# Performance work log

Hardware: AMD Instinct MI355X
Metric: run time of the kernel (lower is better)

## Reference

```python
import jax, jax.numpy as jnp
import numpy as np

P, Q, R = 3, 1, 0          # CliffordAlgebra(p=3, q=1, r=0)
N = P + Q + R
ALG = 1 << N               # 16 basis blades
SHIFTS = (1, 2, 4)


def _cayley():
    """Cayley table C[i,j,k]: blade_i * blade_j = C[i,j,i^j] * blade_{i^j}."""
    metric = [1.0] * P + [-1.0] * Q + [0.0] * R
    C = np.zeros((ALG, ALG, ALG), np.float32)
    for a in range(ALG):
        for b in range(ALG):
            x = a >> 1
            s = 0
            while x:                       # reordering sign
                s += bin(x & b).count('1')
                x >>= 1
            val = -1.0 if (s & 1) else 1.0
            for i in range(N):             # metric for repeated basis vectors
                if (a & b) >> i & 1:
                    val *= metric[i]
            C[a, b, a ^ b] = val
    return C

_C = _cayley()
C0 = jnp.asarray(_C[:, :, 0])                        # grade-0 slice: <a*b>_0
A = jnp.asarray((_C - _C.transpose(1, 0, 2)) / 2.0)  # antisym: (ab - ba)/2
VEC_MASK = jnp.asarray(np.array([1.0 if bin(i).count('1') == 1 else 0.0 for i in range(ALG)], np.float32))
BIV_MASK = jnp.asarray(np.array([1.0 if bin(i).count('1') == 2 else 0.0 for i in range(ALG)], np.float32))


def setup_inputs() -> dict:
    key = jax.random.key(0)
    k1, k2 = jax.random.split(key, 2)
    B, T, D = 8, 4096, 1024
    return {
        "x": jax.random.normal(k1, (B, T, D), jnp.float32),
        "gate_w": jax.random.normal(k2, (D, 1), jnp.float32) * 0.02,
        "gate_b": jnp.zeros((1,), jnp.float32),
        "scalar_weight": jnp.float32(0.5),
        "bivector_weight": jnp.float32(0.5),
    }


def reference(x, gate_w, gate_b, scalar_weight, bivector_weight):
    B, T, D = x.shape
    n = D // ALG                         # 64 chunks of 16 (D divisible, no pad)
    ss = jax.nn.sigmoid(scalar_weight)
    sb = jax.nn.sigmoid(bivector_weight)
    gate = jax.nn.sigmoid(x @ gate_w + gate_b)   # (B,T,1), gate of x (loop-invariant)
    xc = x.reshape(B, T, n, ALG)
    out = x
    for shift in SHIFTS:                 # T=4096 > shift always
        c = x - jnp.roll(x, shift, axis=1)
        cc = c.reshape(B, T, n, ALG)
        # inner product: scalar part per chunk, summed over chunks
        scalar = jnp.einsum('btni,btnj,ij->bt', xc, cc, C0)
        # wedge: antisymmetrized geometric product of vector-grade projections
        av = xc * VEC_MASK
        bv = cc * VEC_MASK
        wedge = jnp.einsum('btni,btnj,ijk->btnk', av, bv, A) * BIV_MASK
        delta = (sb * wedge).reshape(B, T, D)
        delta = delta.at[..., 0].add(ss * scalar)   # scalar_part lives at index 0
        out = out + gate * delta
    return out
```

## Files before the change

### kernel.cpp

```cpp
#include <hip/hip_runtime.h>
#include <math.h>


constexpr int T_DIM = 4096;
constexpr int D_DIM = 1024;

constexpr int QB0 = 0x8000;
constexpr int QB1 = 0x8055;
constexpr int QB2 = 0x80AA;

template <int PAT>
__device__ __forceinline__ float swz(float v) {
    return __int_as_float(__builtin_amdgcn_ds_swizzle(__float_as_int(v), PAT));
}

__device__ __forceinline__ float sigmoidf(float z) {
    return 1.0f / (1.0f + __expf(-z));
}

__global__ __launch_bounds__(256) void clifford_kernel(
    const float* __restrict__ x,
    const float* __restrict__ gate_w,
    const float* __restrict__ gate_b,
    const float* __restrict__ scalar_w,
    const float* __restrict__ bivec_w,
    float* __restrict__ out,
    int BT)
{
    int blk = blockIdx.x;
    if ((gridDim.x & 7) == 0) {
        const int per = gridDim.x >> 3;
        blk = (blockIdx.x & 7) * per + (blockIdx.x >> 3);
    }

    const int lane = threadIdx.x & 63;
    const int row  = blk * 4 + (threadIdx.x >> 6);
    if (row >= BT) return;
    const int b = row >> 12;
    const int t = row & (T_DIM - 1);
    const int sub = lane & 3;

    const float ss = sigmoidf(scalar_w[0]);
    const float sb = sigmoidf(bivec_w[0]);
    const float gb = gate_b[0];

    const float* __restrict__ r0 = x + (size_t)row * D_DIM;
    const size_t brow = (size_t)b * T_DIM;
    const float* __restrict__ r1 = x + (brow + ((t - 1) & (T_DIM - 1))) * D_DIM;
    const float* __restrict__ r2 = x + (brow + ((t - 2) & (T_DIM - 1))) * D_DIM;
    const float* __restrict__ r4 = x + (brow + ((t - 4) & (T_DIM - 1))) * D_DIM;

    float4 ws;
    if      (sub == 0) ws = make_float4( 1.f,  1.f,  1.f, -1.f);
    else if (sub == 1) ws = make_float4( 1.f, -1.f, -1.f, -1.f);
    else if (sub == 2) ws = make_float4(-1.f,  1.f,  1.f,  1.f);
    else               ws = make_float4( 1.f,  1.f,  1.f, -1.f);
    const float m3  = (sub == 0) ? 1.f : 0.f;
    const float a1  = (sub == 1) ? 1.f : 0.f;
    const float a2  = (sub == 2) ? 1.f : 0.f;
    const float m12 = (sub == 3) ? 1.f : 0.f;

    float4 xs[4], dl[4];
    float gate_part = 0.f, sc_part = 0.f;

    #pragma unroll
    for (int m = 0; m < 4; ++m) {
        const int off = (lane << 2) + (m << 8);
        const float4 xv = *(const float4*)(r0 + off);
        const float4 p1 = *(const float4*)(r1 + off);
        const float4 p2 = *(const float4*)(r2 + off);
        const float4 p4 = *(const float4*)(r4 + off);
        const float4 gv = *(const float4*)(gate_w + off);
        xs[m] = xv;

        float4 cs;
        cs.x = 3.f * xv.x - p1.x - p2.x - p4.x;
        cs.y = 3.f * xv.y - p1.y - p2.y - p4.y;
        cs.z = 3.f * xv.z - p1.z - p2.z - p4.z;
        cs.w = 3.f * xv.w - p1.w - p2.w - p4.w;

        gate_part += xv.x * gv.x + xv.y * gv.y + xv.z * gv.z + xv.w * gv.w;
        sc_part   += ws.x * (xv.x * cs.x) + ws.y * (xv.y * cs.y)
                   + ws.z * (xv.z * cs.z) + ws.w * (xv.w * cs.w);

        const float x1 = swz<QB0>(xv.y), x2 = swz<QB0>(xv.z);
        const float x4b = swz<QB1>(xv.x), x8b = swz<QB2>(xv.x);
        const float c1 = swz<QB0>(cs.y), c2 = swz<QB0>(cs.z);
        const float c4b = swz<QB1>(cs.x), c8b = swz<QB2>(cs.x);

        const float w3  = x1 * c2  - x2  * c1;
        const float w5  = x1 * c4b - x4b * c1;
        const float w6  = x2 * c4b - x4b * c2;
        const float w9  = x1 * c8b - x8b * c1;
        const float w10 = x2 * c8b - x8b * c2;
        const float w12 = x4b * c8b - x8b * c4b;

        dl[m] = make_float4(m12 * w12,
                            a1 * w5 + a2 * w9,
                            a1 * w6 + a2 * w10,
                            m3 * w3);
    }

    #pragma unroll
    for (int o = 32; o > 0; o >>= 1) {
        gate_part += __shfl_xor(gate_part, o, 64);
        sc_part   += __shfl_xor(sc_part,   o, 64);
    }
    const float gate = sigmoidf(gate_part + gb);
    const float gsb  = gate * sb;

    float* __restrict__ orow = out + (size_t)row * D_DIM;
    #pragma unroll
    for (int m = 0; m < 4; ++m) {
        float4 o4;
        o4.x = xs[m].x + gsb * dl[m].x;
        o4.y = xs[m].y + gsb * dl[m].y;
        o4.z = xs[m].z + gsb * dl[m].z;
        o4.w = xs[m].w + gsb * dl[m].w;
        if (m == 0 && lane == 0) o4.x += gate * ss * sc_part;
        *(float4*)(orow + (lane << 2) + (m << 8)) = o4;
    }
}

extern "C" void kernel_launch(void* const* d_in, const int* in_sizes, int n_in,
                              void* d_out, int out_size, void* d_ws, size_t ws_size,
                              hipStream_t stream) {
    const float* x  = (const float*)d_in[0];
    const float* gw = (const float*)d_in[1];
    const float* gb = (const float*)d_in[2];
    const float* sw = (const float*)d_in[3];
    const float* bw = (const float*)d_in[4];
    float* out = (float*)d_out;

    const int BT = in_sizes[0] / D_DIM;
    const int blocks = (BT + 3) / 4;
    hipLaunchKernelGGL(clifford_kernel, dim3(blocks), dim3(256), 0, stream,
                       x, gw, gb, sw, bw, out, BT);
}
```

Baseline: 244.9 us.

## Process several consecutive rows per wave with a register ring of prior rows

```diff
diff --git a/kernel.cpp b/kernel.cpp
--- a/kernel.cpp
+++ b/kernel.cpp
@@ -4,6 +4,7 @@
 
 constexpr int T_DIM = 4096;
 constexpr int D_DIM = 1024;
+constexpr int ROWS_PER_WAVE = 8;
 
 constexpr int QB0 = 0x8000;
 constexpr int QB1 = 0x8055;
@@ -18,7 +19,7 @@
     return 1.0f / (1.0f + __expf(-z));
 }
 
-__global__ __launch_bounds__(256) void clifford_kernel(
+__global__ __launch_bounds__(256, 3) void clifford_kernel(
     const float* __restrict__ x,
     const float* __restrict__ gate_w,
     const float* __restrict__ gate_b,
@@ -27,28 +28,34 @@
     float* __restrict__ out,
     int BT)
 {
-    int blk = blockIdx.x;
-    if ((gridDim.x & 7) == 0) {
-        const int per = gridDim.x >> 3;
-        blk = (blockIdx.x & 7) * per + (blockIdx.x >> 3);
+    const int lane = threadIdx.x & 63;
+    const int wid  = blockIdx.x * 4 + (threadIdx.x >> 6);
+    const int r0   = wid * ROWS_PER_WAVE;
+    if (r0 >= BT) return;
+    const int b  = r0 >> 12;
+    const int t0 = r0 & (T_DIM - 1);
+    const size_t brow = (size_t)b * T_DIM;
+    const int sub = lane & 3;
+
+    int off[4];
+    #pragma unroll
+    for (int m = 0; m < 4; ++m) off[m] = (lane << 2) + (m << 8);
+
+    float4 gw4[4];
+    #pragma unroll
+    for (int m = 0; m < 4; ++m) gw4[m] = *(const float4*)(gate_w + off[m]);
+
+    float4 ring[4][4];
+    #pragma unroll
+    for (int k = 1; k <= 4; ++k) {
+        const float* rp = x + (brow + ((t0 - k) & (T_DIM - 1))) * D_DIM;
+        #pragma unroll
+        for (int m = 0; m < 4; ++m) ring[4 - k][m] = *(const float4*)(rp + off[m]);
     }
-
-    const int lane = threadIdx.x & 63;
-    const int row  = blk * 4 + (threadIdx.x >> 6);
-    if (row >= BT) return;
-    const int b = row >> 12;
-    const int t = row & (T_DIM - 1);
-    const int sub = lane & 3;
 
     const float ss = sigmoidf(scalar_w[0]);
     const float sb = sigmoidf(bivec_w[0]);
     const float gb = gate_b[0];
-
-    const float* __restrict__ r0 = x + (size_t)row * D_DIM;
-    const size_t brow = (size_t)b * T_DIM;
-    const float* __restrict__ r1 = x + (brow + ((t - 1) & (T_DIM - 1))) * D_DIM;
-    const float* __restrict__ r2 = x + (brow + ((t - 2) & (T_DIM - 1))) * D_DIM;
-    const float* __restrict__ r4 = x + (brow + ((t - 4) & (T_DIM - 1))) * D_DIM;
 
     float4 ws;
     if      (sub == 0) ws = make_float4( 1.f,  1.f,  1.f, -1.f);
@@ -59,66 +66,82 @@
     const float a1  = (sub == 1) ? 1.f : 0.f;
     const float a2  = (sub == 2) ? 1.f : 0.f;
     const float m12 = (sub == 3) ? 1.f : 0.f;
+    const bool is_lane0 = (lane == 0);
 
-    float4 xs[4], dl[4];
-    float gate_part = 0.f, sc_part = 0.f;
+    const float* __restrict__ xrow = x   + (size_t)r0 * D_DIM;
+    float*       __restrict__ orow = out + (size_t)r0 * D_DIM;
 
-    #pragma unroll
-    for (int m = 0; m < 4; ++m) {
-        const int off = (lane << 2) + (m << 8);
-        const float4 xv = *(const float4*)(r0 + off);
-        const float4 p1 = *(const float4*)(r1 + off);
-        const float4 p2 = *(const float4*)(r2 + off);
-        const float4 p4 = *(const float4*)(r4 + off);
-        const float4 gv = *(const float4*)(gate_w + off);
-        xs[m] = xv;
+    for (int it = 0; it < ROWS_PER_WAVE; it += 4) {
+        #pragma unroll
+        for (int p = 0; p < 4; ++p) {
+            float4 cur[4];
+            #pragma unroll
+            for (int m = 0; m < 4; ++m)
+                cur[m] = *(const float4*)(xrow + off[m]);
 
-        float4 cs;
-        cs.x = 3.f * xv.x - p1.x - p2.x - p4.x;
-        cs.y = 3.f * xv.y - p1.y - p2.y - p4.y;
-        cs.z = 3.f * xv.z - p1.z - p2.z - p4.z;
-        cs.w = 3.f * xv.w - p1.w - p2.w - p4.w;
+            float gate_part = 0.f, sc_part = 0.f;
+            float4 dl[4];
 
-        gate_part += xv.x * gv.x + xv.y * gv.y + xv.z * gv.z + xv.w * gv.w;
-        sc_part   += ws.x * (xv.x * cs.x) + ws.y * (xv.y * cs.y)
-                   + ws.z * (xv.z * cs.z) + ws.w * (xv.w * cs.w);
+            #pragma unroll
+            for (int m = 0; m < 4; ++m) {
+                const float4 xv = cur[m];
+                const float4 p1 = ring[(p + 3) & 3][m];
+                const float4 p2 = ring[(p + 2) & 3][m];
+                const float4 p4 = ring[p & 3][m];
+                float4 cs;
+                cs.x = 3.f * xv.x - p1.x - p2.x - p4.x;
+                cs.y = 3.f * xv.y - p1.y - p2.y - p4.y;
+                cs.z = 3.f * xv.z - p1.z - p2.z - p4.z;
+                cs.w = 3.f * xv.w - p1.w - p2.w - p4.w;
 
-        const float x1 = swz<QB0>(xv.y), x2 = swz<QB0>(xv.z);
-        const float x4b = swz<QB1>(xv.x), x8b = swz<QB2>(xv.x);
-        const float c1 = swz<QB0>(cs.y), c2 = swz<QB0>(cs.z);
-        const float c4b = swz<QB1>(cs.x), c8b = swz<QB2>(cs.x);
+                gate_part += xv.x * gw4[m].x + xv.y * gw4[m].y
+                           + xv.z * gw4[m].z + xv.w * gw4[m].w;
+                sc_part   += ws.x * (xv.x * cs.x) + ws.y * (xv.y * cs.y)
+                           + ws.z * (xv.z * cs.z) + ws.w * (xv.w * cs.w);
 
-        const float w3  = x1 * c2  - x2  * c1;
-        const float w5  = x1 * c4b - x4b * c1;
-        const float w6  = x2 * c4b - x4b * c2;
-        const float w9  = x1 * c8b - x8b * c1;
-        const float w10 = x2 * c8b - x8b * c2;
-        const float w12 = x4b * c8b - x8b * c4b;
+                const float x1  = swz<QB0>(xv.y), x2  = swz<QB0>(xv.z);
+                const float x4b = swz<QB1>(xv.x), x8b = swz<QB2>(xv.x);
+                const float c1  = swz<QB0>(cs.y), c2  = swz<QB0>(cs.z);
+                const float c4b = swz<QB1>(cs.x), c8b = swz<QB2>(cs.x);
 
-        dl[m] = make_float4(m12 * w12,
-                            a1 * w5 + a2 * w9,
-                            a1 * w6 + a2 * w10,
-                            m3 * w3);
-    }
+                const float w3  = x1 * c2  - x2  * c1;
+                const float w5  = x1 * c4b - x4b * c1;
+                const float w6  = x2 * c4b - x4b * c2;
+                const float w9  = x1 * c8b - x8b * c1;
+                const float w10 = x2 * c8b - x8b * c2;
+                const float w12 = x4b * c8b - x8b * c4b;
 
-    #pragma unroll
-    for (int o = 32; o > 0; o >>= 1) {
-        gate_part += __shfl_xor(gate_part, o, 64);
-        sc_part   += __shfl_xor(sc_part,   o, 64);
-    }
-    const float gate = sigmoidf(gate_part + gb);
-    const float gsb  = gate * sb;
+                dl[m] = make_float4(m12 * w12,
+                                    a1 * w5 + a2 * w9,
+                                    a1 * w6 + a2 * w10,
+                                    m3 * w3);
+            }
 
-    float* __restrict__ orow = out + (size_t)row * D_DIM;
-    #pragma unroll
-    for (int m = 0; m < 4; ++m) {
-        float4 o4;
-        o4.x = xs[m].x + gsb * dl[m].x;
-        o4.y = xs[m].y + gsb * dl[m].y;
-        o4.z = xs[m].z + gsb * dl[m].z;
-        o4.w = xs[m].w + gsb * dl[m].w;
-        if (m == 0 && lane == 0) o4.x += gate * ss * sc_part;
-        *(float4*)(orow + (lane << 2) + (m << 8)) = o4;
+            #pragma unroll
+            for (int o = 32; o > 0; o >>= 1) {
+                gate_part += __shfl_xor(gate_part, o, 64);
+                sc_part   += __shfl_xor(sc_part,   o, 64);
+            }
+            const float gate = sigmoidf(gate_part + gb);
+            const float gsb  = gate * sb;
+
+            #pragma unroll
+            for (int m = 0; m < 4; ++m) {
+                float4 o4;
+                o4.x = cur[m].x + gsb * dl[m].x;
+                o4.y = cur[m].y + gsb * dl[m].y;
+                o4.z = cur[m].z + gsb * dl[m].z;
+                o4.w = cur[m].w + gsb * dl[m].w;
+                if (m == 0 && is_lane0) o4.x += gate * ss * sc_part;
+                *(float4*)(orow + off[m]) = o4;
+            }
+
+            #pragma unroll
+            for (int m = 0; m < 4; ++m) ring[p & 3][m] = cur[m];
+
+            xrow += D_DIM;
+            orow += D_DIM;
+        }
     }
 }
 
@@ -133,7 +156,8 @@
     float* out = (float*)d_out;
 
     const int BT = in_sizes[0] / D_DIM;
-    const int blocks = (BT + 3) / 4;
+    const int waves = (BT + ROWS_PER_WAVE - 1) / ROWS_PER_WAVE;
+    const int blocks = (waves + 3) / 4;
     hipLaunchKernelGGL(clifford_kernel, dim3(blocks), dim3(256), 0, stream,
                        x, gw, gb, sw, bw, out, BT);
 }
```

Result: slower. 256.3 us (+4.7%).

## Stage row tile with halo in LDS via direct global-to-LDS loads

Applied to the files above, without the earlier changes.

```diff
diff --git a/kernel.cpp b/kernel.cpp
--- a/kernel.cpp
+++ b/kernel.cpp
@@ -4,6 +4,9 @@
 
 constexpr int T_DIM = 4096;
 constexpr int D_DIM = 1024;
+constexpr int HALO = 4;
+constexpr int ROWS_PER_BLOCK = 4;
+constexpr int TILE_ROWS = ROWS_PER_BLOCK + HALO;
 
 constexpr int QB0 = 0x8000;
 constexpr int QB1 = 0x8055;
@@ -18,7 +21,7 @@
     return 1.0f / (1.0f + __expf(-z));
 }
 
-__global__ __launch_bounds__(256) void clifford_kernel(
+__global__ __launch_bounds__(256, 4) void clifford_kernel(
     const float* __restrict__ x,
     const float* __restrict__ gate_w,
     const float* __restrict__ gate_b,
@@ -27,6 +30,8 @@
     float* __restrict__ out,
     int BT)
 {
+    __shared__ __align__(16) float tile[TILE_ROWS * D_DIM];
+
     int blk = blockIdx.x;
     if ((gridDim.x & 7) == 0) {
         const int per = gridDim.x >> 3;
@@ -34,44 +39,65 @@
     }
 
     const int lane = threadIdx.x & 63;
-    const int row  = blk * 4 + (threadIdx.x >> 6);
-    if (row >= BT) return;
-    const int b = row >> 12;
-    const int t = row & (T_DIM - 1);
+    const int w    = threadIdx.x >> 6;
+    const int r0   = blk * ROWS_PER_BLOCK;
+    if (r0 >= BT) return;
+    const int b  = r0 >> 12;
+    const int t0 = r0 & (T_DIM - 1);
+    const size_t brow = (size_t)b * T_DIM;
     const int sub = lane & 3;
 
+    #pragma unroll
+    for (int r = 0; r < 8; ++r) {
+        const int s    = r * 4 + w;
+        const int lr   = s >> 2;
+        const int part = s & 3;
+        const int t    = (t0 - HALO + lr) & (T_DIM - 1);
+        const float* g = x + (brow + t) * (size_t)D_DIM + part * 256 + lane * 4;
+        __builtin_amdgcn_global_load_lds(
+            (const __attribute__((address_space(1))) unsigned int*)g,
+            (__attribute__((address_space(3))) unsigned int*)(tile + s * 256),
+            16, 0, 0);
+    }
+
+    float4 gv[4];
+    #pragma unroll
+    for (int m = 0; m < 4; ++m)
+        gv[m] = *(const float4*)(gate_w + lane * 4 + m * 256);
     const float ss = sigmoidf(scalar_w[0]);
     const float sb = sigmoidf(bivec_w[0]);
     const float gb = gate_b[0];
 
-    const float* __restrict__ r0 = x + (size_t)row * D_DIM;
-    const size_t brow = (size_t)b * T_DIM;
-    const float* __restrict__ r1 = x + (brow + ((t - 1) & (T_DIM - 1))) * D_DIM;
-    const float* __restrict__ r2 = x + (brow + ((t - 2) & (T_DIM - 1))) * D_DIM;
-    const float* __restrict__ r4 = x + (brow + ((t - 4) & (T_DIM - 1))) * D_DIM;
-
-    float4 ws;
-    if      (sub == 0) ws = make_float4( 1.f,  1.f,  1.f, -1.f);
-    else if (sub == 1) ws = make_float4( 1.f, -1.f, -1.f, -1.f);
-    else if (sub == 2) ws = make_float4(-1.f,  1.f,  1.f,  1.f);
-    else               ws = make_float4( 1.f,  1.f,  1.f, -1.f);
+    float4 wsg;
+    if      (sub == 0) wsg = make_float4( 1.f,  1.f,  1.f, -1.f);
+    else if (sub == 1) wsg = make_float4( 1.f, -1.f, -1.f, -1.f);
+    else if (sub == 2) wsg = make_float4(-1.f,  1.f,  1.f,  1.f);
+    else               wsg = make_float4( 1.f,  1.f,  1.f, -1.f);
     const float m3  = (sub == 0) ? 1.f : 0.f;
     const float a1  = (sub == 1) ? 1.f : 0.f;
     const float a2  = (sub == 2) ? 1.f : 0.f;
     const float m12 = (sub == 3) ? 1.f : 0.f;
 
-    float4 xs[4], dl[4];
+    __syncthreads();
+
+    const float4* __restrict__ t4 = (const float4*)tile;
+    const int lr = HALO + w;
+    const int b0 = lr * 256;
+    const int b1 = (lr - 1) * 256;
+    const int b2 = (lr - 2) * 256;
+    const int b4 = (lr - 4) * 256;
+
     float gate_part = 0.f, sc_part = 0.f;
+    float4 cur[4], dl[4];
 
     #pragma unroll
     for (int m = 0; m < 4; ++m) {
-        const int off = (lane << 2) + (m << 8);
-        const float4 xv = *(const float4*)(r0 + off);
-        const float4 p1 = *(const float4*)(r1 + off);
-        const float4 p2 = *(const float4*)(r2 + off);
-        const float4 p4 = *(const float4*)(r4 + off);
-        const float4 gv = *(const float4*)(gate_w + off);
-        xs[m] = xv;
+        const int e = m * 64 + lane;
+        const float4 xv = t4[b0 + e];
+        const float4 p1 = t4[b1 + e];
+        const float4 p2 = t4[b2 + e];
+        const float4 p4 = t4[b4 + e];
+        cur[m] = xv;
 
         float4 cs;
         cs.x = 3.f * xv.x - p1.x - p2.x - p4.x;
@@ -79,13 +105,14 @@
         cs.z = 3.f * xv.z - p1.z - p2.z - p4.z;
         cs.w = 3.f * xv.w - p1.w - p2.w - p4.w;
 
-        gate_part += xv.x * gv.x + xv.y * gv.y + xv.z * gv.z + xv.w * gv.w;
-        sc_part   += ws.x * (xv.x * cs.x) + ws.y * (xv.y * cs.y)
-                   + ws.z * (xv.z * cs.z) + ws.w * (xv.w * cs.w);
+        gate_part += xv.x * gv[m].x + xv.y * gv[m].y
+                   + xv.z * gv[m].z + xv.w * gv[m].w;
+        sc_part   += wsg.x * (xv.x * cs.x) + wsg.y * (xv.y * cs.y)
+                   + wsg.z * (xv.z * cs.z) + wsg.w * (xv.w * cs.w);
 
-        const float x1 = swz<QB0>(xv.y), x2 = swz<QB0>(xv.z);
+        const float x1  = swz<QB0>(xv.y), x2  = swz<QB0>(xv.z);
         const float x4b = swz<QB1>(xv.x), x8b = swz<QB2>(xv.x);
-        const float c1 = swz<QB0>(cs.y), c2 = swz<QB0>(cs.z);
+        const float c1  = swz<QB0>(cs.y), c2  = swz<QB0>(cs.z);
         const float c4b = swz<QB1>(cs.x), c8b = swz<QB2>(cs.x);
 
         const float w3  = x1 * c2  - x2  * c1;
@@ -109,16 +136,16 @@
     const float gate = sigmoidf(gate_part + gb);
     const float gsb  = gate * sb;
 
-    float* __restrict__ orow = out + (size_t)row * D_DIM;
+    float* __restrict__ orow = out + (size_t)(r0 + w) * D_DIM;
     #pragma unroll
     for (int m = 0; m < 4; ++m) {
         float4 o4;
-        o4.x = xs[m].x + gsb * dl[m].x;
-        o4.y = xs[m].y + gsb * dl[m].y;
-        o4.z = xs[m].z + gsb * dl[m].z;
-        o4.w = xs[m].w + gsb * dl[m].w;
+        o4.x = cur[m].x + gsb * dl[m].x;
+        o4.y = cur[m].y + gsb * dl[m].y;
+        o4.z = cur[m].z + gsb * dl[m].z;
+        o4.w = cur[m].w + gsb * dl[m].w;
         if (m == 0 && lane == 0) o4.x += gate * ss * sc_part;
-        *(float4*)(orow + (lane << 2) + (m << 8)) = o4;
+        *(float4*)(orow + lane * 4 + m * 256) = o4;
     }
 }
 
@@ -133,7 +160,7 @@
     float* out = (float*)d_out;
 
     const int BT = in_sizes[0] / D_DIM;
-    const int blocks = (BT + 3) / 4;
+    const int blocks = (BT + ROWS_PER_BLOCK - 1) / ROWS_PER_BLOCK;
     hipLaunchKernelGGL(clifford_kernel, dim3(blocks), dim3(256), 0, stream,
                        x, gw, gb, sw, bw, out, BT);
 }
```

New measurement: 242.3 us. About the same (-1.1%).
